# Kernel optimization log

Measured on AMD Instinct MI355X. Metric: run time of the kernel, lower is better.

## Reference

```python
import jax, jax.numpy as jnp
import numpy as np

B, L, S, D, H, E, UV = 4, 2048, 2048, 1024, 8, 128, 128
ROT_DIM = H * E  # RotaryEmbedding(dim=qk_size*n_heads) applied on flattened dim


def gelu(x):
    return jax.nn.gelu(x, approximate=False)  # torch nn.GELU default (erf)


def rope(x):
    # x: [B, T, ROT_DIM]; interleaved-pair rotary (lucidrains rotary_embedding_torch default)
    T = x.shape[1]
    inv_freq = 1.0 / (10000.0 ** (jnp.arange(0, ROT_DIM, 2, dtype=jnp.float32) / ROT_DIM))
    freqs = jnp.arange(T, dtype=jnp.float32)[:, None] * inv_freq  # [T, ROT_DIM/2]
    cos = jnp.repeat(jnp.cos(freqs), 2, axis=-1)  # [T, ROT_DIM]
    sin = jnp.repeat(jnp.sin(freqs), 2, axis=-1)
    xp = x.reshape(*x.shape[:-1], ROT_DIM // 2, 2)
    x_rot = jnp.stack([-xp[..., 1], xp[..., 0]], axis=-1).reshape(x.shape)
    return x * cos + x_rot * sin


def setup_inputs() -> dict:
    key = jax.random.key(0)
    ks = jax.random.split(key, 16)
    n = lambda k, sh, s=1.0: jax.random.normal(k, sh, jnp.float32) * s
    w = 0.02
    return {
        "u": n(ks[0], (B, L, D)),
        "queries": n(ks[1], (B, L, D)),
        "keys": n(ks[2], (B, S, D)),
        "values": n(ks[3], (B, S, D)),
        "Wqk": n(ks[4], (D, H * E), w), "bqk": jnp.zeros((H * E,), jnp.float32),
        "Wv": n(ks[5], (D, H * UV), w), "bv": jnp.zeros((H * UV,), jnp.float32),
        "Wu": n(ks[6], (D, H * UV), w), "bu": jnp.zeros((H * UV,), jnp.float32),
        "Wo": n(ks[7], (H * UV, D), w), "bo": jnp.zeros((D,), jnp.float32),
        "q_gamma": jnp.ones((E,), jnp.float32), "q_beta": n(ks[8], (E,), w),
        "k_gamma": jnp.ones((E,), jnp.float32), "k_beta": n(ks[9], (E,), w),
    }


def _forward(u, queries, keys, values, Wqk, bqk, Wv, bv, Wu, bu, Wo, bo,
             q_gamma, q_beta, k_gamma, k_beta):
    # use_aff=True: shared qk projection + per-branch ScaleOffset over qk_size
    qk = gelu(queries @ Wqk + bqk)                      # [B,L,H*E]
    qk4 = qk.reshape(B, L, H, E)
    q = (qk4 * q_gamma + q_beta).reshape(B, L, H * E)
    k = (qk4 * k_gamma + k_beta).reshape(B, L, H * E)
    q = rope(q).reshape(B, L, H, E)
    k = rope(k).reshape(B, S, H, E)
    v = gelu(values @ Wv + bv).reshape(B, S, H, UV)
    # Conv1d(kernel_size=1) == pointwise linear over channels
    u_p = gelu(u @ Wu + bu).reshape(B, L, H, UV)
    scale = 1.0 / jnp.sqrt(jnp.float32(E))
    scores = jnp.einsum("blhe,bshe->bhls", q, k) * scale
    attn = jax.nn.softmax(scores, axis=-1)              # [B,H,L,S]
    ctx = jnp.einsum("bhls,bshd->blhd", attn, v)        # [B,L,H,UV]
    out = (u_p * ctx).reshape(B, L, H * UV)             # gate by u
    o = out @ Wo + bo                                   # [B,L,D]
    return o, attn


def reference(u, queries, keys, values, Wqk, bqk, Wv, bv, Wu, bu, Wo, bo,
              q_gamma, q_beta, k_gamma, k_beta):
    return _forward(u, queries, keys, values, Wqk, bqk, Wv, bv, Wu, bu, Wo, bo,
                    q_gamma, q_beta, k_gamma, k_beta)
```

## Files before the change

### kernel.cpp

```cpp
#include <hip/hip_runtime.h>
#include <hip/hip_bf16.h>
#include <math.h>

#define DEVI static __device__ __forceinline__

typedef __attribute__((ext_vector_type(4))) float f32x4;
typedef __attribute__((ext_vector_type(16))) float f32x16;
typedef __attribute__((ext_vector_type(8))) short bf16x8;
typedef __attribute__((ext_vector_type(4))) short bf16x4;

constexpr int Bc = 4, Lc = 2048, Sc = 2048, Dc = 1024, Hc = 8, Ec = 128, UVc = 128;
constexpr int HEc = Hc * Ec;
constexpr int BLc = Bc * Lc;

#define QSC (1.44269504088896340f / 11.31370849898476039f)

DEVI unsigned f2bf_bits(float f) {
  unsigned u = __builtin_bit_cast(unsigned, f);
  return (u + 0x7FFFu + ((u >> 16) & 1u)) >> 16;
}
DEVI short f2bf(float f) { return (short)f2bf_bits(f); }
DEVI float bf2f(short s) {
  return __builtin_bit_cast(float, (unsigned)((unsigned short)s) << 16);
}
DEVI float gelu_f(float x) {
  float z = fabsf(x) * 0.7071067811865476f;
  float t = __builtin_amdgcn_rcpf(1.0f + 0.3275911f * z);
  float p = t * (0.254829592f +
            t * (-0.284496736f +
            t * (1.421413741f +
            t * (-1.453152027f + t * 1.061405429f))));
  float e = exp2f(-z * z * 1.4426950408889634f);
  float er = copysignf(1.0f - p * e, x);
  return 0.5f * x * (1.0f + er);
}

DEVI void gload16(const void* gsrc, void* ldst) {
  __builtin_amdgcn_global_load_lds(
      (const __attribute__((address_space(1))) unsigned*)gsrc,
      (__attribute__((address_space(3))) unsigned*)(ldst), 16, 0, 0);
}

DEVI f32x4 mfma16(bf16x8 a, bf16x8 b, f32x4 c) {
  return __builtin_amdgcn_mfma_f32_16x16x32_bf16(a, b, c, 0, 0, 0);
}
DEVI f32x16 mfma32(bf16x8 a, bf16x8 b, f32x16 c) {
  return __builtin_amdgcn_mfma_f32_32x32x16_bf16(a, b, c, 0, 0, 0);
}

__global__ void prep_all_kernel(const float* __restrict__ in_q, const float* __restrict__ in_v,
                                const float* __restrict__ in_u, short* __restrict__ C1,
                                short* __restrict__ C2, short* __restrict__ C3,
                                const float* __restrict__ W0, const float* __restrict__ W1,
                                const float* __restrict__ W2, const float* __restrict__ W3,
                                short* __restrict__ T0, short* __restrict__ T1,
                                short* __restrict__ T2, short* __restrict__ T3,
                                float2* __restrict__ cs) {
  __shared__ float tbuf[32][33];
  const int bid = blockIdx.x;
  const int t = threadIdx.x;
  if (bid < 12288) {
    int which = bid >> 12, blk = bid & 4095;
    const float* in = (which == 0) ? in_q : (which == 1) ? in_v : in_u;
    short* out = (which == 0) ? C1 : (which == 1) ? C2 : C3;
    size_t i = ((size_t)blk * 256 + t) * 8;
    float4 f1 = *reinterpret_cast<const float4*>(in + i);
    float4 f2 = *reinterpret_cast<const float4*>(in + i + 4);
    uint4 pk;
    pk.x = f2bf_bits(f1.x) | (f2bf_bits(f1.y) << 16);
    pk.y = f2bf_bits(f1.z) | (f2bf_bits(f1.w) << 16);
    pk.z = f2bf_bits(f2.x) | (f2bf_bits(f2.y) << 16);
    pk.w = f2bf_bits(f2.z) | (f2bf_bits(f2.w) << 16);
    *reinterpret_cast<uint4*>(out + i) = pk;
  } else if (bid < 17408) {
    int z = (bid - 12288) >> 10, rem = (bid - 12288) & 1023;
    int n0 = (rem & 31) * 32, k0 = (rem >> 5) * 32;
    int tx = t & 31, ty = t >> 5;
    const float* Ws[4] = {W0, W1, W2, W3};
    short* Ts[4] = {T0, T1, T2, T3};
    const float* W = Ws[z];
    short* WT = Ts[z];
#pragma unroll
    for (int i = 0; i < 4; i++) {
      int r = ty + i * 8;
      tbuf[r][tx] = W[(size_t)(k0 + r) * 1024 + n0 + tx];
    }
    __syncthreads();
#pragma unroll
    for (int i = 0; i < 4; i++) {
      int r = ty + i * 8;
      WT[(size_t)(n0 + r) * 1024 + k0 + tx] = f2bf(tbuf[tx][r]);
    }
  } else {
    int base = (bid - 17408) * 256 + t;
#pragma unroll
    for (int j = 0; j < 4; j++) {
      int idx = base + j * 262144;
      int tt = idx >> 9, i = idx & 511;
      float inv = expf((float)i * (-9.210340371976184f / 512.0f));
      float sv, cv;
      sincosf((float)tt * inv, &sv, &cv);
      cs[idx] = make_float2(cv, sv);
    }
  }
}

#define GEMM_MAIN_LOOP(A, BT, K)                                                     \
  const int tid = threadIdx.x;                                                       \
  const int wave = tid >> 6, lane = tid & 63;                                        \
  const int lquad = lane >> 4, l15 = lane & 15;                                      \
  const int m0 = blockIdx.x * 128, n0 = blockIdx.y * 128;                            \
  const int wr = wave >> 1, wc = wave & 1;                                           \
  f32x4 acc[4][4] = {};                                                              \
  const int q0 = tid * 16, q1 = tid * 16 + 4096;                                     \
  const int r0 = q0 >> 6, o0 = (q0 & 63) ^ ((r0 & 3) << 4);                          \
  const int r1 = q1 >> 6, o1 = (q1 & 63) ^ ((r1 & 3) << 4);                          \
  const short* a0 = (A) + (size_t)(m0 + r0) * (K) + (o0 >> 1);                       \
  const short* a1 = (A) + (size_t)(m0 + r1) * (K) + (o1 >> 1);                       \
  const short* b0 = (BT) + (size_t)(n0 + r0) * (K) + (o0 >> 1);                      \
  const short* b1 = (BT) + (size_t)(n0 + r1) * (K) + (o1 >> 1);                      \
  G_STAGE(0, 0);                                                                     \
  G_STAGE(1, 32);                                                                    \
  asm volatile("s_waitcnt vmcnt(4)" ::: "memory");                                   \
  __builtin_amdgcn_s_barrier();                                                      \
  const int NT = (K) >> 5;                                                           \
  int cur = 0;                                                                       \
  for (int t = 0; t < NT; t++) {                                                     \
    int nb = cur + 2;                                                                \
    if (nb >= 3) nb -= 3;                                                            \
    G_STAGE(nb, (t + 2 < NT) ? (t + 2) * 32 : 0);                                    \
    __builtin_amdgcn_sched_barrier(0);                                               \
    const char* As_ = smem + cur * 8192;                                             \
    const char* Bs_ = smem + 24576 + cur * 8192;                                     \
    const int ko = lquad * 16;                                                       \
    bf16x8 a[4], b[4];                                                               \
    _Pragma("unroll") for (int f = 0; f < 4; f++) {                                  \
      int ra = wr * 64 + f * 16 + l15;                                               \
      a[f] = *reinterpret_cast<const bf16x8*>(As_ + ra * 64 + (ko ^ ((ra & 3) << 4)));\
      int rb = wc * 64 + f * 16 + l15;                                               \
      b[f] = *reinterpret_cast<const bf16x8*>(Bs_ + rb * 64 + (ko ^ ((rb & 3) << 4)));\
    }                                                                                \
    _Pragma("unroll") for (int mf = 0; mf < 4; mf++)                                 \
      _Pragma("unroll") for (int nf = 0; nf < 4; nf++)                               \
        acc[mf][nf] = mfma16(a[mf], b[nf], acc[mf][nf]);                             \
    asm volatile("s_waitcnt vmcnt(4) lgkmcnt(0)" ::: "memory");                      \
    __builtin_amdgcn_sched_barrier(0);                                               \
    __builtin_amdgcn_s_barrier();                                                    \
    cur = (cur == 2) ? 0 : cur + 1;                                                  \
  }

#define G_STAGE(buf, kt)                     \
  {                                          \
    char* As_ = smem + (buf)*8192;           \
    char* Bs_ = smem + 24576 + (buf)*8192;   \
    gload16(a0 + (kt), As_ + q0);            \
    gload16(a1 + (kt), As_ + q1);            \
    gload16(b0 + (kt), Bs_ + q0);            \
    gload16(b1 + (kt), Bs_ + q1);            \
  }

template <int EPI>
__global__ __launch_bounds__(256, 3) void gemm_kernel(
    const short* __restrict__ A, const short* __restrict__ BT,
    const float* __restrict__ bias, void* __restrict__ Cptr, int M, int N, int K) {
  __shared__ char smem[49152];
  GEMM_MAIN_LOOP(A, BT, K)
#pragma unroll
  for (int mf = 0; mf < 4; mf++) {
#pragma unroll
    for (int nf = 0; nf < 4; nf++) {
      const int mrow = m0 + wr * 64 + mf * 16 + 4 * lquad;
      const int ncol = n0 + wc * 64 + nf * 16 + l15;
      const float bval = bias[ncol];
      if constexpr (EPI == 3) {
        int hh = ncol >> 7, dd = ncol & 127;
        int bb = mrow >> 11, ss = mrow & 2047;
        bf16x4 gv;
#pragma unroll
        for (int r = 0; r < 4; r++) gv[r] = f2bf(gelu_f(acc[mf][nf][r] + bval));
        *reinterpret_cast<bf16x4*>((short*)Cptr + (((size_t)bb * 8 + hh) * 128 + dd) * 2048 + ss) = gv;
      } else if constexpr (EPI == 1) {
#pragma unroll
        for (int r = 0; r < 4; r++)
          ((short*)Cptr)[(size_t)(mrow + r) * N + ncol] = f2bf(gelu_f(acc[mf][nf][r] + bval));
      } else {
#pragma unroll
        for (int r = 0; r < 4; r++)
          ((float*)Cptr)[(size_t)(mrow + r) * N + ncol] = acc[mf][nf][r] + bval;
      }
    }
  }
}

__global__ __launch_bounds__(256, 3) void gemm_rope_kernel(
    const short* __restrict__ A, const short* __restrict__ BT,
    const float* __restrict__ bias, const float2* __restrict__ cstab,
    const float* __restrict__ qg, const float* __restrict__ qb,
    const float* __restrict__ kg, const float* __restrict__ kb,
    short* __restrict__ qout, short* __restrict__ kout) {
  __shared__ char smem[49152];
  GEMM_MAIN_LOOP(A, BT, Dc)
#pragma unroll
  for (int mf = 0; mf < 4; mf++) {
#pragma unroll
    for (int nf = 0; nf < 4; nf++) {
      const int mrow = m0 + wr * 64 + mf * 16 + 4 * lquad;
      const int ncol = n0 + wc * 64 + nf * 16 + l15;
      const float bval = bias[ncol];
      const int e7 = ncol & 127;
      const float QG = qg[e7], QB = qb[e7], KG = kg[e7], KB = kb[e7];
      const int p = ncol >> 1;
      const float sgn = (ncol & 1) ? 1.0f : -1.0f;
#pragma unroll
      for (int r = 0; r < 4; r++) {
        const int m = mrow + r;
        const int tt = m & 2047;
        float2 cs = cstab[(size_t)tt * 512 + p];
        float g = gelu_f(acc[mf][nf][r] + bval);
        float qv = g * QG + QB, kv = g * KG + KB;
        float pq = __shfl_xor(qv, 1), pk = __shfl_xor(kv, 1);
        qout[(size_t)m * HEc + ncol] = f2bf((qv * cs.x + sgn * pq * cs.y) * QSC);
        kout[(size_t)m * HEc + ncol] = f2bf(kv * cs.x + sgn * pk * cs.y);
      }
    }
  }
}
#undef G_STAGE
#undef GEMM_MAIN_LOOP

__global__ __launch_bounds__(256, 3) void passa_kernel(
    const short* __restrict__ qs, const short* __restrict__ ks,
    float* __restrict__ rcpbuf) {
  __shared__ char smem[49152];
  const int bid = blockIdx.x;
  const int xcd = bid & 7, jj = bid >> 3;
  const int bh = xcd * 4 + (jj >> 4);
  const int lblk = jj & 15;
  const int b = bh >> 3, h = bh & 7;
  const int l0 = lblk * 128;
  const int tid = threadIdx.x;
  const int wave = tid >> 6, lane = tid & 63;
  const int l31 = lane & 31, lhg = lane >> 5;

  const short* ksrc[4];
  int kq[4];
#pragma unroll
  for (int i = 0; i < 4; i++) {
    int q = i * 4096 + tid * 16;
    kq[i] = q;
    int row = q >> 8, off = (q & 255) ^ ((row & 7) << 4);
    ksrc[i] = ks + (((size_t)b * Sc + row) * Hc + h) * Ec + (off >> 1);
  }

  bf16x8 qf[8];
  {
    const char* qp = (const char*)(qs + (((size_t)b * Lc + l0 + wave * 32 + l31) * Hc + h) * Ec);
#pragma unroll
    for (int kt = 0; kt < 8; kt++)
      qf[kt] = *reinterpret_cast<const bf16x8*>(qp + kt * 32 + 16 * lhg);
  }
  __builtin_amdgcn_sched_barrier(0);

#define STAGE_A(buf, s0)                                  \
  {                                                       \
    char* Kb_ = smem + (buf)*16384;                       \
    gload16(ksrc[0] + (size_t)(s0)*1024, Kb_ + kq[0]);    \
    gload16(ksrc[1] + (size_t)(s0)*1024, Kb_ + kq[1]);    \
    gload16(ksrc[2] + (size_t)(s0)*1024, Kb_ + kq[2]);    \
    gload16(ksrc[3] + (size_t)(s0)*1024, Kb_ + kq[3]);    \
  }

  STAGE_A(0, 0);
  STAGE_A(1, 64);
  asm volatile("s_waitcnt vmcnt(4)" ::: "memory");
  __builtin_amdgcn_s_barrier();
  float ra = 0.f, rb = 0.f, rc = 0.f, rd = 0.f;
  int cur = 0;
  for (int t = 0; t < 32; t++) {
    int nb = cur + 2;
    if (nb >= 3) nb -= 3;
    STAGE_A(nb, (t + 2 < 32) ? (t + 2) * 64 : 0);
    __builtin_amdgcn_sched_barrier(0);
    const char* KB_ = smem + cur * 16384;
    f32x16 d0 = {}, d1 = {};
    __builtin_amdgcn_s_setprio(1);
#pragma unroll
    for (int kt = 0; kt < 8; kt++) {
      int row0 = l31, row1 = 32 + l31;
      bf16x8 k0 = *reinterpret_cast<const bf16x8*>(
          KB_ + row0 * 256 + ((kt * 32 + 16 * lhg) ^ ((row0 & 7) << 4)));
      bf16x8 k1 = *reinterpret_cast<const bf16x8*>(
          KB_ + row1 * 256 + ((kt * 32 + 16 * lhg) ^ ((row1 & 7) << 4)));
      d0 = mfma32(k0, qf[kt], d0);
      d1 = mfma32(k1, qf[kt], d1);
    }
    __builtin_amdgcn_s_setprio(0);
#pragma unroll
    for (int r = 0; r < 16; r += 4) {
      ra += exp2f(d0[r]) + exp2f(d1[r]);
      rb += exp2f(d0[r + 1]) + exp2f(d1[r + 1]);
      rc += exp2f(d0[r + 2]) + exp2f(d1[r + 2]);
      rd += exp2f(d0[r + 3]) + exp2f(d1[r + 3]);
    }
    asm volatile("s_waitcnt vmcnt(4) lgkmcnt(0)" ::: "memory");
    __builtin_amdgcn_sched_barrier(0);
    __builtin_amdgcn_s_barrier();
    cur = (cur == 2) ? 0 : cur + 1;
  }
#undef STAGE_A
  float rs = (ra + rb) + (rc + rd);
  rs += __shfl_xor(rs, 32);
  if (lane < 32)
    rcpbuf[(size_t)bh * Lc + l0 + wave * 32 + l31] = 1.0f / rs;
}

__global__ __launch_bounds__(256, 3) void attn_kernel(
    const short* __restrict__ qs, const short* __restrict__ ks,
    const short* __restrict__ vT, const short* __restrict__ up,
    const float* __restrict__ rcpbuf, float* __restrict__ attn_out,
    short* __restrict__ gate) {
  __shared__ char smem[49152];
  const int bid = blockIdx.x;
  const int xcd = bid & 7, jj = bid >> 3;
  const int bh = xcd * 4 + (jj >> 4);
  const int lblk = jj & 15;
  const int b = bh >> 3, h = bh & 7;
  const int l0 = lblk * 128;
  const int tid = threadIdx.x;
  const int wave = tid >> 6, lane = tid & 63;
  const int lquad = lane >> 4, l15 = lane & 15;

  const short* ksrc[2];
  int kq[2];
#pragma unroll
  for (int i = 0; i < 2; i++) {
    int q = i * 4096 + tid * 16;
    kq[i] = q;
    int row = q >> 8, off = (q & 255) ^ ((row & 7) << 4);
    ksrc[i] = ks + (((size_t)b * Sc + row) * Hc + h) * Ec + (off >> 1);
  }
  const short* vsrc[2];
  int vq[2];
#pragma unroll
  for (int i = 0; i < 2; i++) {
    int q = i * 4096 + tid * 16;
    vq[i] = q;
    int rv = q >> 6;
    int j = (q >> 4) & 3;
    int c = (j - (rv & 3)) & 3;
    vsrc[i] = vT + ((size_t)bh * UVc + rv) * Sc + (c << 3);
  }

  bf16x8 qf[2][4];
  float rcp[2];
#pragma unroll
  for (int cf = 0; cf < 2; cf++) {
    int lrow = l0 + wave * 32 + cf * 16 + l15;
    const short* qp = qs + (((size_t)b * Lc + lrow) * Hc + h) * Ec;
#pragma unroll
    for (int kt = 0; kt < 4; kt++)
      qf[cf][kt] = *reinterpret_cast<const bf16x8*>(qp + kt * 32 + lquad * 8);
    rcp[cf] = rcpbuf[(size_t)bh * Lc + lrow];
  }
  __builtin_amdgcn_sched_barrier(0);

#define STAGE_B(buf, s0)                                  \
  {                                                       \
    char* Kb_ = smem + (buf)*8192;                        \
    char* Vb_ = smem + 24576 + (buf)*8192;                \
    gload16(ksrc[0] + (size_t)(s0)*1024, Kb_ + kq[0]);    \
    gload16(ksrc[1] + (size_t)(s0)*1024, Kb_ + kq[1]);    \
    gload16(vsrc[0] + (s0), Vb_ + vq[0]);                 \
    gload16(vsrc[1] + (s0), Vb_ + vq[1]);                 \
  }

  STAGE_B(0, 0);
  STAGE_B(1, 32);
  asm volatile("s_waitcnt vmcnt(4)" ::: "memory");
  __builtin_amdgcn_s_barrier();
  f32x4 ctx[8][2] = {};
  int cur = 0;
  for (int t = 0; t < 64; t++) {
    const int s0 = t * 32;
    const char* KB_ = smem + cur * 8192;
    const char* VB_ = smem + 24576 + cur * 8192;
    f32x4 d[2][2] = {};
    __builtin_amdgcn_s_setprio(1);
#pragma unroll
    for (int kt = 0; kt < 4; kt++)
#pragma unroll
      for (int sf = 0; sf < 2; sf++) {
        int row = sf * 16 + l15;
        bf16x8 kf = *reinterpret_cast<const bf16x8*>(
            KB_ + row * 256 + ((kt * 64 + lquad * 16) ^ ((row & 7) << 4)));
        d[sf][0] = mfma16(kf, qf[0][kt], d[sf][0]);
        d[sf][1] = mfma16(kf, qf[1][kt], d[sf][1]);
      }
    __builtin_amdgcn_s_setprio(0);
#pragma unroll
    for (int sf = 0; sf < 2; sf++)
#pragma unroll
      for (int cf = 0; cf < 2; cf++)
#pragma unroll
        for (int r = 0; r < 4; r++)
          d[sf][cf][r] = exp2f(d[sf][cf][r]) * rcp[cf];
#pragma unroll
    for (int cf = 0; cf < 2; cf++) {
      int lrow = l0 + wave * 32 + cf * 16 + l15;
      float* arow = attn_out + ((size_t)bh * Lc + lrow) * Sc + s0 + lquad * 4;
      __builtin_nontemporal_store(d[0][cf], reinterpret_cast<f32x4*>(arow));
      __builtin_nontemporal_store(d[1][cf], reinterpret_cast<f32x4*>(arow + 16));
    }
    bf16x8 pb[2];
#pragma unroll
    for (int cf = 0; cf < 2; cf++)
#pragma unroll
      for (int r = 0; r < 4; r++) {
        pb[cf][r] = f2bf(d[0][cf][r]);
        pb[cf][4 + r] = f2bf(d[1][cf][r]);
      }
    __builtin_amdgcn_s_setprio(1);
#pragma unroll
    for (int df = 0; df < 8; df++) {
      int dd = df * 16 + l15;
      const char* vrow = VB_ + dd * 64;
      int half = (lquad & 1) * 8;
      int clo = ((lquad >> 1) + (dd & 3)) & 3;
      int chi = ((lquad >> 1) + 2 + (dd & 3)) & 3;
      bf16x4 lo = *reinterpret_cast<const bf16x4*>(vrow + clo * 16 + half);
      bf16x4 hi = *reinterpret_cast<const bf16x4*>(vrow + chi * 16 + half);
      bf16x8 vf = __builtin_shufflevector(lo, hi, 0, 1, 2, 3, 4, 5, 6, 7);
      ctx[df][0] = mfma16(vf, pb[0], ctx[df][0]);
      ctx[df][1] = mfma16(vf, pb[1], ctx[df][1]);
    }
    __builtin_amdgcn_s_setprio(0);
    {
      int nb = cur + 2;
      if (nb >= 3) nb -= 3;
      STAGE_B(nb, (t + 2 < 64) ? s0 + 64 : 0);
    }
    asm volatile("s_waitcnt vmcnt(8) lgkmcnt(0)" ::: "memory");
    __builtin_amdgcn_sched_barrier(0);
    __builtin_amdgcn_s_barrier();
    cur = (cur == 2) ? 0 : cur + 1;
  }
#undef STAGE_B

#pragma unroll
  for (int cf = 0; cf < 2; cf++) {
    int lrow = l0 + wave * 32 + cf * 16 + l15;
    size_t base = ((size_t)b * Lc + lrow) * HEc + h * UVc;
    const short* ub = up + base;
    short* gp = gate + base;
#pragma unroll
    for (int df = 0; df < 8; df++) {
      int doff = df * 16 + lquad * 4;
      bf16x4 uv = *reinterpret_cast<const bf16x4*>(ub + doff);
      bf16x4 gv;
#pragma unroll
      for (int r = 0; r < 4; r++)
        gv[r] = f2bf(bf2f(uv[r]) * ctx[df][cf][r]);
      *reinterpret_cast<bf16x4*>(gp + doff) = gv;
    }
  }
}

extern "C" void kernel_launch(void* const* d_in, const int* in_sizes, int n_in,
                              void* d_out, int out_size, void* d_ws, size_t ws_size,
                              hipStream_t stream) {
  const float* u_in = (const float*)d_in[0];
  const float* qry = (const float*)d_in[1];
  const float* vals = (const float*)d_in[3];
  const float* Wqk = (const float*)d_in[4];
  const float* bqk = (const float*)d_in[5];
  const float* Wv = (const float*)d_in[6];
  const float* bv = (const float*)d_in[7];
  const float* Wu = (const float*)d_in[8];
  const float* bu = (const float*)d_in[9];
  const float* Wo = (const float*)d_in[10];
  const float* bo = (const float*)d_in[11];
  const float* qg = (const float*)d_in[12];
  const float* qb = (const float*)d_in[13];
  const float* kg = (const float*)d_in[14];
  const float* kb = (const float*)d_in[15];

  char* w = (char*)d_ws;
  short* WT0 = (short*)w; w += (size_t)1024 * 1024 * 2;
  short* WT1 = (short*)w; w += (size_t)1024 * 1024 * 2;
  short* WT2 = (short*)w; w += (size_t)1024 * 1024 * 2;
  short* WT3 = (short*)w; w += (size_t)1024 * 1024 * 2;
  float2* cstab = (float2*)w; w += (size_t)2048 * 512 * 8;
  float* rcpb = (float*)w; w += (size_t)32 * 2048 * 4;
  const size_t BUF = (size_t)BLc * HEc * 2;
  short* C1 = (short*)w; w += BUF;
  short* C2 = (short*)w; w += BUF;
  short* C3 = (short*)w; w += BUF;
  short* qbf = (short*)w; w += BUF;
  short* kbf = (short*)w; w += BUF;
  short* vTb = (short*)w; w += BUF;
  short* upb = (short*)w; w += BUF;
  short* gtb = C1;

  float* o_out = (float*)d_out;
  float* attn_out = o_out + (size_t)BLc * Dc;

  prep_all_kernel<<<18432, 256, 0, stream>>>(qry, vals, u_in, C1, C2, C3, Wqk, Wv, Wu, Wo,
                                             WT0, WT1, WT2, WT3, cstab);
  gemm_rope_kernel<<<dim3(64, 8), 256, 0, stream>>>(C1, WT0, bqk, cstab, qg, qb, kg, kb,
                                                    qbf, kbf);
  passa_kernel<<<512, 256, 0, stream>>>(qbf, kbf, rcpb);
  gemm_kernel<3><<<dim3(64, 8), 256, 0, stream>>>(C2, WT1, bv, vTb, BLc, HEc, Dc);
  gemm_kernel<1><<<dim3(64, 8), 256, 0, stream>>>(C3, WT2, bu, upb, BLc, HEc, Dc);
  attn_kernel<<<512, 256, 0, stream>>>(qbf, kbf, vTb, upb, rcpb, attn_out, gtb);
  gemm_kernel<0><<<dim3(64, 8), 256, 0, stream>>>(gtb, WT3, bo, o_out, BLc, Dc, HEc);
}
```

Baseline: 378.8 us.

## Merge softmax-denominator pass and V/U projection GEMMs into one launch

The row-sum pass (passa) and the two independent V and U projection GEMMs are merged into a single heterogeneous kernel that dispatches on block index, so the three run concurrently within one launch. The GEMM code moves from a macro into a templated device function shared by all GEMM kernels, and the grids become 1D. The aim is to fill the GPU better and cut launch gaps and tail effects between small kernels. The trade-off is mixed workloads per CU and register pressure set by the heaviest branch.

```diff
diff --git a/kernel.cpp b/kernel.cpp
--- a/kernel.cpp
+++ b/kernel.cpp
@@ -105,49 +105,28 @@
   }
 }
 
-#define GEMM_MAIN_LOOP(A, BT, K)                                                     \
-  const int tid = threadIdx.x;                                                       \
-  const int wave = tid >> 6, lane = tid & 63;                                        \
-  const int lquad = lane >> 4, l15 = lane & 15;                                      \
-  const int m0 = blockIdx.x * 128, n0 = blockIdx.y * 128;                            \
-  const int wr = wave >> 1, wc = wave & 1;                                           \
-  f32x4 acc[4][4] = {};                                                              \
-  const int q0 = tid * 16, q1 = tid * 16 + 4096;                                     \
-  const int r0 = q0 >> 6, o0 = (q0 & 63) ^ ((r0 & 3) << 4);                          \
-  const int r1 = q1 >> 6, o1 = (q1 & 63) ^ ((r1 & 3) << 4);                          \
-  const short* a0 = (A) + (size_t)(m0 + r0) * (K) + (o0 >> 1);                       \
-  const short* a1 = (A) + (size_t)(m0 + r1) * (K) + (o1 >> 1);                       \
-  const short* b0 = (BT) + (size_t)(n0 + r0) * (K) + (o0 >> 1);                      \
-  const short* b1 = (BT) + (size_t)(n0 + r1) * (K) + (o1 >> 1);                      \
-  G_STAGE(0, 0);                                                                     \
-  G_STAGE(1, 32);                                                                    \
-  asm volatile("s_waitcnt vmcnt(4)" ::: "memory");                                   \
-  __builtin_amdgcn_s_barrier();                                                      \
-  const int NT = (K) >> 5;                                                           \
-  int cur = 0;                                                                       \
-  for (int t = 0; t < NT; t++) {                                                     \
-    int nb = cur + 2;                                                                \
-    if (nb >= 3) nb -= 3;                                                            \
-    G_STAGE(nb, (t + 2 < NT) ? (t + 2) * 32 : 0);                                    \
-    __builtin_amdgcn_sched_barrier(0);                                               \
-    const char* As_ = smem + cur * 8192;                                             \
-    const char* Bs_ = smem + 24576 + cur * 8192;                                     \
-    const int ko = lquad * 16;                                                       \
-    bf16x8 a[4], b[4];                                                               \
-    _Pragma("unroll") for (int f = 0; f < 4; f++) {                                  \
-      int ra = wr * 64 + f * 16 + l15;                                               \
-      a[f] = *reinterpret_cast<const bf16x8*>(As_ + ra * 64 + (ko ^ ((ra & 3) << 4)));\
-      int rb = wc * 64 + f * 16 + l15;                                               \
-      b[f] = *reinterpret_cast<const bf16x8*>(Bs_ + rb * 64 + (ko ^ ((rb & 3) << 4)));\
-    }                                                                                \
-    _Pragma("unroll") for (int mf = 0; mf < 4; mf++)                                 \
-      _Pragma("unroll") for (int nf = 0; nf < 4; nf++)                               \
-        acc[mf][nf] = mfma16(a[mf], b[nf], acc[mf][nf]);                             \
-    asm volatile("s_waitcnt vmcnt(4) lgkmcnt(0)" ::: "memory");                      \
-    __builtin_amdgcn_sched_barrier(0);                                               \
-    __builtin_amdgcn_s_barrier();                                                    \
-    cur = (cur == 2) ? 0 : cur + 1;                                                  \
-  }
+template <int EPI>
+DEVI void gemm_body(char* smem, int bx,
+                    const short* __restrict__ A, const short* __restrict__ BT,
+                    const float* __restrict__ bias, void* __restrict__ Cptr, int K, int N,
+                    const float2* __restrict__ cstab,
+                    const float* __restrict__ qg, const float* __restrict__ qb,
+                    const float* __restrict__ kg, const float* __restrict__ kb,
+                    short* __restrict__ qout, short* __restrict__ kout) {
+  const int tid = threadIdx.x;
+  const int wave = tid >> 6, lane = tid & 63;
+  const int lquad = lane >> 4, l15 = lane & 15;
+  const int m0 = (bx & 63) * 128, n0 = (bx >> 6) * 128;
+  const int wr = wave >> 1, wc = wave & 1;
+  f32x4 acc[4][4] = {};
+
+  const int q0 = tid * 16, q1 = tid * 16 + 4096;
+  const int r0 = q0 >> 6, o0 = (q0 & 63) ^ ((r0 & 3) << 4);
+  const int r1 = q1 >> 6, o1 = (q1 & 63) ^ ((r1 & 3) << 4);
+  const short* a0 = A + (size_t)(m0 + r0) * K + (o0 >> 1);
+  const short* a1 = A + (size_t)(m0 + r1) * K + (o1 >> 1);
+  const short* b0 = BT + (size_t)(n0 + r0) * K + (o0 >> 1);
+  const short* b1 = BT + (size_t)(n0 + r1) * K + (o1 >> 1);
 
 #define G_STAGE(buf, kt)                     \
   {                                          \
@@ -159,12 +138,41 @@
     gload16(b1 + (kt), Bs_ + q1);            \
   }
 
-template <int EPI>
-__global__ __launch_bounds__(256, 3) void gemm_kernel(
-    const short* __restrict__ A, const short* __restrict__ BT,
-    const float* __restrict__ bias, void* __restrict__ Cptr, int M, int N, int K) {
-  __shared__ char smem[49152];
-  GEMM_MAIN_LOOP(A, BT, K)
+  G_STAGE(0, 0);
+  G_STAGE(1, 32);
+  asm volatile("s_waitcnt vmcnt(4)" ::: "memory");
+  __builtin_amdgcn_s_barrier();
+
+  const int NT = K >> 5;
+  int cur = 0;
+  for (int t = 0; t < NT; t++) {
+    int nb = cur + 2;
+    if (nb >= 3) nb -= 3;
+    G_STAGE(nb, (t + 2 < NT) ? (t + 2) * 32 : 0);
+    __builtin_amdgcn_sched_barrier(0);
+    const char* As_ = smem + cur * 8192;
+    const char* Bs_ = smem + 24576 + cur * 8192;
+    const int ko = lquad * 16;
+    bf16x8 a[4], b[4];
+#pragma unroll
+    for (int f = 0; f < 4; f++) {
+      int ra = wr * 64 + f * 16 + l15;
+      a[f] = *reinterpret_cast<const bf16x8*>(As_ + ra * 64 + (ko ^ ((ra & 3) << 4)));
+      int rb = wc * 64 + f * 16 + l15;
+      b[f] = *reinterpret_cast<const bf16x8*>(Bs_ + rb * 64 + (ko ^ ((rb & 3) << 4)));
+    }
+#pragma unroll
+    for (int mf = 0; mf < 4; mf++)
+#pragma unroll
+      for (int nf = 0; nf < 4; nf++)
+        acc[mf][nf] = mfma16(a[mf], b[nf], acc[mf][nf]);
+    asm volatile("s_waitcnt vmcnt(4) lgkmcnt(0)" ::: "memory");
+    __builtin_amdgcn_sched_barrier(0);
+    __builtin_amdgcn_s_barrier();
+    cur = (cur == 2) ? 0 : cur + 1;
+  }
+#undef G_STAGE
+
 #pragma unroll
   for (int mf = 0; mf < 4; mf++) {
 #pragma unroll
@@ -172,7 +180,23 @@
       const int mrow = m0 + wr * 64 + mf * 16 + 4 * lquad;
       const int ncol = n0 + wc * 64 + nf * 16 + l15;
       const float bval = bias[ncol];
-      if constexpr (EPI == 3) {
+      if constexpr (EPI == 2) {
+        const int e7 = ncol & 127;
+        const float QG = qg[e7], QB = qb[e7], KG = kg[e7], KB = kb[e7];
+        const int p = ncol >> 1;
+        const float sgn = (ncol & 1) ? 1.0f : -1.0f;
+#pragma unroll
+        for (int r = 0; r < 4; r++) {
+          const int m = mrow + r;
+          const int tt = m & 2047;
+          float2 cs = cstab[(size_t)tt * 512 + p];
+          float g = gelu_f(acc[mf][nf][r] + bval);
+          float qv = g * QG + QB, kv = g * KG + KB;
+          float pq = __shfl_xor(qv, 1), pk = __shfl_xor(kv, 1);
+          qout[(size_t)m * HEc + ncol] = f2bf((qv * cs.x + sgn * pq * cs.y) * QSC);
+          kout[(size_t)m * HEc + ncol] = f2bf(kv * cs.x + sgn * pk * cs.y);
+        }
+      } else if constexpr (EPI == 3) {
         int hh = ncol >> 7, dd = ncol & 127;
         int bb = mrow >> 11, ss = mrow & 2047;
         bf16x4 gv;
@@ -192,47 +216,8 @@
   }
 }
 
-__global__ __launch_bounds__(256, 3) void gemm_rope_kernel(
-    const short* __restrict__ A, const short* __restrict__ BT,
-    const float* __restrict__ bias, const float2* __restrict__ cstab,
-    const float* __restrict__ qg, const float* __restrict__ qb,
-    const float* __restrict__ kg, const float* __restrict__ kb,
-    short* __restrict__ qout, short* __restrict__ kout) {
-  __shared__ char smem[49152];
-  GEMM_MAIN_LOOP(A, BT, Dc)
-#pragma unroll
-  for (int mf = 0; mf < 4; mf++) {
-#pragma unroll
-    for (int nf = 0; nf < 4; nf++) {
-      const int mrow = m0 + wr * 64 + mf * 16 + 4 * lquad;
-      const int ncol = n0 + wc * 64 + nf * 16 + l15;
-      const float bval = bias[ncol];
-      const int e7 = ncol & 127;
-      const float QG = qg[e7], QB = qb[e7], KG = kg[e7], KB = kb[e7];
-      const int p = ncol >> 1;
-      const float sgn = (ncol & 1) ? 1.0f : -1.0f;
-#pragma unroll
-      for (int r = 0; r < 4; r++) {
-        const int m = mrow + r;
-        const int tt = m & 2047;
-        float2 cs = cstab[(size_t)tt * 512 + p];
-        float g = gelu_f(acc[mf][nf][r] + bval);
-        float qv = g * QG + QB, kv = g * KG + KB;
-        float pq = __shfl_xor(qv, 1), pk = __shfl_xor(kv, 1);
-        qout[(size_t)m * HEc + ncol] = f2bf((qv * cs.x + sgn * pq * cs.y) * QSC);
-        kout[(size_t)m * HEc + ncol] = f2bf(kv * cs.x + sgn * pk * cs.y);
-      }
-    }
-  }
-}
-#undef G_STAGE
-#undef GEMM_MAIN_LOOP
-
-__global__ __launch_bounds__(256, 3) void passa_kernel(
-    const short* __restrict__ qs, const short* __restrict__ ks,
-    float* __restrict__ rcpbuf) {
-  __shared__ char smem[49152];
-  const int bid = blockIdx.x;
+DEVI void passa_body(char* smem, int bid, const short* __restrict__ qs,
+                     const short* __restrict__ ks, float* __restrict__ rcpbuf) {
   const int xcd = bid & 7, jj = bid >> 3;
   const int bh = xcd * 4 + (jj >> 4);
   const int lblk = jj & 15;
@@ -312,6 +297,44 @@
   rs += __shfl_xor(rs, 32);
   if (lane < 32)
     rcpbuf[(size_t)bh * Lc + l0 + wave * 32 + l31] = 1.0f / rs;
+}
+
+__global__ __launch_bounds__(256, 3) void mid_kernel(
+    const short* __restrict__ qs, const short* __restrict__ ks, float* __restrict__ rcpbuf,
+    const short* __restrict__ C2, const short* __restrict__ WT1,
+    const float* __restrict__ bv, short* __restrict__ vTb,
+    const short* __restrict__ C3, const short* __restrict__ WT2,
+    const float* __restrict__ bu, short* __restrict__ upb) {
+  __shared__ char smem[49152];
+  const int bid = blockIdx.x;
+  if (bid < 512) {
+    passa_body(smem, bid, qs, ks, rcpbuf);
+  } else if (bid < 1024) {
+    gemm_body<3>(smem, bid - 512, C2, WT1, bv, vTb, Dc, HEc,
+                 nullptr, nullptr, nullptr, nullptr, nullptr, nullptr, nullptr);
+  } else {
+    gemm_body<1>(smem, bid - 1024, C3, WT2, bu, upb, Dc, HEc,
+                 nullptr, nullptr, nullptr, nullptr, nullptr, nullptr, nullptr);
+  }
+}
+
+__global__ __launch_bounds__(256, 3) void gemm_rope_kernel(
+    const short* __restrict__ A, const short* __restrict__ BT,
+    const float* __restrict__ bias, const float2* __restrict__ cstab,
+    const float* __restrict__ qg, const float* __restrict__ qb,
+    const float* __restrict__ kg, const float* __restrict__ kb,
+    short* __restrict__ qout, short* __restrict__ kout) {
+  __shared__ char smem[49152];
+  gemm_body<2>(smem, blockIdx.x, A, BT, bias, nullptr, Dc, HEc,
+               cstab, qg, qb, kg, kb, qout, kout);
+}
+
+__global__ __launch_bounds__(256, 3) void gemm_out_kernel(
+    const short* __restrict__ A, const short* __restrict__ BT,
+    const float* __restrict__ bias, float* __restrict__ C) {
+  __shared__ char smem[49152];
+  gemm_body<0>(smem, blockIdx.x, A, BT, bias, C, HEc, Dc,
+               nullptr, nullptr, nullptr, nullptr, nullptr, nullptr, nullptr);
 }
 
 __global__ __launch_bounds__(256, 3) void attn_kernel(
@@ -506,11 +529,8 @@
 
   prep_all_kernel<<<18432, 256, 0, stream>>>(qry, vals, u_in, C1, C2, C3, Wqk, Wv, Wu, Wo,
                                              WT0, WT1, WT2, WT3, cstab);
-  gemm_rope_kernel<<<dim3(64, 8), 256, 0, stream>>>(C1, WT0, bqk, cstab, qg, qb, kg, kb,
-                                                    qbf, kbf);
-  passa_kernel<<<512, 256, 0, stream>>>(qbf, kbf, rcpb);
-  gemm_kernel<3><<<dim3(64, 8), 256, 0, stream>>>(C2, WT1, bv, vTb, BLc, HEc, Dc);
-  gemm_kernel<1><<<dim3(64, 8), 256, 0, stream>>>(C3, WT2, bu, upb, BLc, HEc, Dc);
+  gemm_rope_kernel<<<512, 256, 0, stream>>>(C1, WT0, bqk, cstab, qg, qb, kg, kb, qbf, kbf);
+  mid_kernel<<<1536, 256, 0, stream>>>(qbf, kbf, rcpb, C2, WT1, bv, vTb, C3, WT2, bu, upb);
   attn_kernel<<<512, 256, 0, stream>>>(qbf, kbf, vTb, upb, rcpb, attn_out, gtb);
-  gemm_kernel<0><<<dim3(64, 8), 256, 0, stream>>>(gtb, WT3, bo, o_out, BLc, Dc, HEc);
-}
+  gemm_out_kernel<<<512, 256, 0, stream>>>(gtb, WT3, bo, o_out);
+}
```

Result: faster. 365.0 us (-3.7%).
